# Kernel tuning notes

Hardware: AMD Instinct MI355X
Metric: run time of the kernel (lower is better)

Reference implementation:

```python
import jax, jax.numpy as jnp
import numpy as np
from jax import lax

EPS = 1e-5  # clamp floor used in both quantizers (matches torch clamp_(min=1e-05))


def activation_quant(x):
    # per-token (per n,h,w across channel dim=1) 8-bit fake quant
    scale = 127.0 / jnp.clip(jnp.max(jnp.abs(x), axis=1, keepdims=True), EPS, None)
    return jnp.clip(jnp.round(x * scale), -128.0, 127.0) / scale


def weight_quant(w):
    # per-tensor ternary (1.58-bit) fake quant
    scale = 1.0 / jnp.clip(jnp.mean(jnp.abs(w)), EPS, None)
    return jnp.clip(jnp.round(w * scale), -1.0, 1.0) / scale


def setup_inputs() -> dict:
    key = jax.random.key(0)
    kx, kw, kb = jax.random.split(key, 3)
    N, Cin, H, W = 16, 64, 256, 256
    Cout, kh, kw_ = 64, 3, 3
    x = jax.random.normal(kx, (N, Cin, H, W), dtype=jnp.float32)
    fan_in = Cin * kh * kw_
    # kaiming-uniform-like init scale
    bound = np.sqrt(6.0 / fan_in)
    weight = jax.random.uniform(kw, (Cout, Cin, kh, kw_), dtype=jnp.float32,
                                minval=-bound, maxval=bound)
    bias = jnp.zeros((Cout,), dtype=jnp.float32)
    return {"x": x, "weight": weight, "bias": bias}


def reference(x, weight, bias):
    # straight-through estimator: value = quantized, grad flows through identity
    dqx = x - lax.stop_gradient(x - activation_quant(x))
    dqw = weight - lax.stop_gradient(weight - weight_quant(weight))
    out = lax.conv_general_dilated(
        dqx, dqw,
        window_strides=(1, 1),
        padding=((1, 1), (1, 1)),
        lhs_dilation=(1, 1),
        rhs_dilation=(1, 1),
        dimension_numbers=("NCHW", "OIHW", "NCHW"),
        feature_group_count=1,
    )
    return out + bias[None, :, None, None]
```

## Files before the change

### kernel.cpp

```cpp
#include <hip/hip_runtime.h>
#include <hip/hip_bf16.h>

typedef __attribute__((ext_vector_type(8))) short short8;
typedef __attribute__((ext_vector_type(4))) float f32x4;
typedef __attribute__((ext_vector_type(4))) int i32x4;
typedef unsigned short u16;
typedef unsigned int u32;
typedef __attribute__((ext_vector_type(8))) unsigned short u16x8;
typedef __attribute__((ext_vector_type(4))) u32 u32x4;

#define XN 16
#define XC 64
#define XH 256
#define XW 256
#define XO 64
#define CH_STRIDE (XH * XW)

#define QX_OFF    0
#define INVS_OFF  67108864
#define WBUF_OFF  71303168
#define PART_OFF  71340032
#define WM_OFF    71340288
#define WS_NEED   71340544

__global__ __launch_bounds__(256) void wq_reduce(const float* __restrict__ w,
                                                 float* __restrict__ partials) {
    __shared__ float red[4];
    const int tid = threadIdx.x;
    const int base = blockIdx.x * 576;
    float s = 0.f;
    for (int i = tid; i < 576; i += 256) s += fabsf(w[base + i]);
    #pragma unroll
    for (int off = 32; off > 0; off >>= 1) s += __shfl_down(s, off, 64);
    if ((tid & 63) == 0) red[tid >> 6] = s;
    __syncthreads();
    if (tid == 0) partials[blockIdx.x] = red[0] + red[1] + red[2] + red[3];
}

__global__ __launch_bounds__(256) void wq_tern_i8(const float* __restrict__ w,
                                                  const float* __restrict__ partials,
                                                  float* __restrict__ wm_out,
                                                  signed char* __restrict__ wbuf) {
    __shared__ float wm_sh;
    const int tid = threadIdx.x;
    if (tid == 0) {
        float tot = 0.f;
        #pragma unroll
        for (int i = 0; i < 64; ++i) tot += partials[i];
        float wm = fmaxf(tot / (float)(XO * XC * 9), 1e-5f);
        wm_sh = wm;
        if (blockIdx.x == 0) wm_out[0] = wm;
    }
    __syncthreads();
    const float wscale = 1.0f / wm_sh;

    const int idx = blockIdx.x * 256 + tid;
    const int j = idx & 15;
    const int l = (idx >> 4) & 63;
    const int m = (idx >> 10) & 3;
    const int t = idx >> 12;
    const int o = m * 16 + (l & 15);
    const int i = (l >> 4) * 16 + j;
    const int kh = t / 3, kw = t % 3;
    const float wv = w[((o * XC + i) * 3 + kh) * 3 + kw];
    const float tern = fminf(fmaxf(rintf(wv * wscale), -1.f), 1.f);
    wbuf[idx] = (signed char)(int)tern;
}

__global__ __launch_bounds__(256) void aq_i8(const float* __restrict__ x,
                                             signed char* __restrict__ qx,
                                             float* __restrict__ invs) {
    const int tid = threadIdx.x;
    const int b = blockIdx.x;
    const int n = b >> 8;

    const float* px = x + ((size_t)n << 22) + ((size_t)(b & 255) << 8) + tid;
    float vals[64];
    float amax = 0.f;
    #pragma unroll
    for (int c = 0; c < 64; ++c) {
        const float v = px[(size_t)c << 16];
        vals[c] = v;
        amax = fmaxf(amax, fabsf(v));
    }
    const float am = fmaxf(amax, 1e-5f);
    const float scale = 127.0f / am;
    invs[((size_t)b << 8) + tid] = am * (1.0f / 127.0f);

    u32 words[16];
    #pragma unroll
    for (int wk = 0; wk < 16; ++wk) {
        u32 acc = 0;
        #pragma unroll
        for (int bb = 0; bb < 4; ++bb) {
            const float q = fminf(fmaxf(rintf(vals[wk * 4 + bb] * scale), -128.f), 127.f);
            acc |= ((u32)((int)q) & 255u) << (bb * 8);
        }
        words[wk] = acc;
    }
    u32* dst = (u32*)(qx + ((((size_t)b << 8) + tid) << 6));
    #pragma unroll
    for (int i = 0; i < 4; ++i) {
        *reinterpret_cast<u32x4*>(dst + i * 4) =
            (u32x4){words[i * 4], words[i * 4 + 1], words[i * 4 + 2], words[i * 4 + 3]};
    }
}

__global__ __launch_bounds__(256, 3) void conv_i8(const signed char* __restrict__ qx,
                                                  const float* __restrict__ invs,
                                                  const signed char* __restrict__ wbuf,
                                                  const float* __restrict__ wm_ptr,
                                                  const float* __restrict__ bias,
                                                  float* __restrict__ out) {
    const int tid = threadIdx.x;
    const int bid = (blockIdx.x & 7) * 1024 + (blockIdx.x >> 3);
    const int n      = bid >> 9;
    const int rem    = bid & 511;
    const int rowgrp = rem >> 3;
    const int w0     = (rem & 7) << 5;
    const int wv     = tid >> 6;
    const int gh_out = (rowgrp << 2) + wv;
    const int lane = tid & 63;
    const int l15 = lane & 15;
    const int lg  = lane >> 4;

    const float wm = wm_ptr[0];

    const signed char* qn = qx + ((size_t)n << 22);
    const float*       in = invs + ((size_t)n << 16);

    int gwc[2][3]; bool cok[2][3];
    #pragma unroll
    for (int nt = 0; nt < 2; ++nt)
        #pragma unroll
        for (int dw = 0; dw < 3; ++dw) {
            const int gw = w0 + nt * 16 + l15 + dw - 1;
            cok[nt][dw] = (gw >= 0) & (gw < XW);
            gwc[nt][dw] = min(max(gw, 0), XW - 1);
        }

    i32x4 B[9][2];
    float IV[9][2];
    #pragma unroll
    for (int dh = 0; dh < 3; ++dh) {
        const int gh = gh_out + dh - 1;
        const bool rok = (gh >= 0) & (gh < XH);
        const int ghc = min(max(gh, 0), XH - 1);
        const signed char* qrow = qn + ((size_t)ghc << 14);
        const float*       irow = in + (ghc << 8);
        #pragma unroll
        for (int dw = 0; dw < 3; ++dw) {
            #pragma unroll
            for (int nt = 0; nt < 2; ++nt) {
                const int c = gwc[nt][dw];
                B[dh * 3 + dw][nt] =
                    *reinterpret_cast<const i32x4*>(qrow + (c << 6) + (lg << 4));
                IV[dh * 3 + dw][nt] = (rok & cok[nt][dw]) ? irow[c] : 0.f;
            }
        }
    }
    __builtin_amdgcn_sched_barrier(0);

    f32x4 acc[4][2];
    #pragma unroll
    for (int m = 0; m < 4; ++m) {
        acc[m][0] = (f32x4){0.f, 0.f, 0.f, 0.f};
        acc[m][1] = (f32x4){0.f, 0.f, 0.f, 0.f};
    }

    #pragma unroll
    for (int t = 0; t < 9; ++t) {
        #pragma unroll
        for (int m = 0; m < 4; ++m) {
            const i32x4 af = *reinterpret_cast<const i32x4*>(
                wbuf + (((t << 2) + m) << 10) + (lane << 4));
            #pragma unroll
            for (int nt = 0; nt < 2; ++nt) {
                i32x4 tap = __builtin_amdgcn_mfma_i32_16x16x64_i8(
                    af, B[t][nt], (i32x4){0, 0, 0, 0}, 0, 0, 0);
                f32x4 tf;
                tf[0] = (float)tap[0]; tf[1] = (float)tap[1];
                tf[2] = (float)tap[2]; tf[3] = (float)tap[3];
                acc[m][nt] += tf * IV[t][nt];
            }
        }
    }

    #pragma unroll
    for (int m = 0; m < 4; ++m) {
        #pragma unroll
        for (int r = 0; r < 4; ++r) {
            const int o = (m << 4) + (lg << 2) + r;
            const float bz = bias[o];
            float* orow = out + ((((size_t)n << 6) + o) << 16) + (gh_out << 8) + w0;
            __builtin_nontemporal_store(fmaf(acc[m][0][r], wm, bz), orow + l15);
            __builtin_nontemporal_store(fmaf(acc[m][1][r], wm, bz), orow + 16 + l15);
        }
    }
}

#define HALO_W 34
#define NPIX 340

__global__ __launch_bounds__(256) void wq_kernel(const float* __restrict__ w,
                                                 float* __restrict__ wm_out,
                                                 u16* __restrict__ wbuf) {
    __shared__ float red[4];
    __shared__ float wm_sh;
    const int tid = threadIdx.x;

    float s = 0.f;
    for (int i = tid; i < XO * XC * 9; i += 256) s += fabsf(w[i]);
    #pragma unroll
    for (int off = 32; off > 0; off >>= 1) s += __shfl_down(s, off, 64);
    if ((tid & 63) == 0) red[tid >> 6] = s;
    __syncthreads();
    if (tid == 0) {
        float tot = red[0] + red[1] + red[2] + red[3];
        float wm = fmaxf(tot / (float)(XO * XC * 9), 1e-5f);
        wm_out[0] = wm;
        wm_sh = wm;
    }
    __syncthreads();
    const float wscale = 1.0f / wm_sh;

    for (int idx = tid; idx < XO * XC * 9; idx += 256) {
        const int j = idx & 7;
        const int l = (idx >> 3) & 63;
        const int c = (idx >> 9) & 1;
        const int m = (idx >> 10) & 3;
        const int t = idx >> 12;
        const int o = m * 16 + (l & 15);
        const int i = c * 32 + (l >> 4) * 8 + j;
        const int kh = t / 3, kw = t % 3;
        const float wv = w[((o * XC + i) * 3 + kh) * 3 + kw];
        const float tern = fminf(fmaxf(rintf(wv * wscale), -1.f), 1.f);
        wbuf[idx] = (u16)(__float_as_uint(tern) >> 16);
    }
}

__global__ __launch_bounds__(256) void conv_kernel(const float* __restrict__ x,
                                                   const u16* __restrict__ wbuf,
                                                   const float* __restrict__ wm_ptr,
                                                   const float* __restrict__ bias,
                                                   float* __restrict__ out) {
    __shared__ __align__(16) u16 q_lds[NPIX * 64];
    __shared__ float invs_lds[NPIX];
    __shared__ float bias_lds[XO];

    const int tid = threadIdx.x;
    const int bid = blockIdx.x;
    const int n   = bid >> 8;
    const int rem = bid & 255;
    const int h0  = (rem >> 3) << 3;
    const int w0  = (rem & 7) << 5;

    if (tid < XO) bias_lds[tid] = bias[tid];

    #pragma unroll 1
    for (int p = tid; p < NPIX; p += 256) {
        const int hr = p / HALO_W;
        const int cl = p - hr * HALO_W;
        const int gh = h0 + hr - 1;
        const int gw = w0 + cl - 1;
        const bool ok = (gh >= 0) & (gh < XH) & (gw >= 0) & (gw < XW);

        float vals[64];
        float amax = 0.f;
        if (ok) {
            const float* px = x + (size_t)n * (XC * CH_STRIDE) + (size_t)gh * XW + gw;
            #pragma unroll
            for (int c = 0; c < 64; ++c) {
                const float v = px[(size_t)c * CH_STRIDE];
                vals[c] = v;
                amax = fmaxf(amax, fabsf(v));
            }
        } else {
            #pragma unroll
            for (int c = 0; c < 64; ++c) vals[c] = 0.f;
        }
        const float am    = fmaxf(amax, 1e-5f);
        const float scale = 127.0f / am;
        invs_lds[p] = ok ? (1.0f / scale) : 0.0f;

        const int sw = (p & 7) << 3;
        #pragma unroll
        for (int cb = 0; cb < 8; ++cb) {
            u16x8 pk;
            #pragma unroll
            for (int j = 0; j < 8; ++j) {
                const float q = fminf(fmaxf(rintf(vals[cb * 8 + j] * scale), -128.f), 127.f);
                pk[j] = (u16)(__float_as_uint(q) >> 16);
            }
            *reinterpret_cast<u16x8*>(&q_lds[p * 64 + ((cb * 8) ^ sw)]) = pk;
        }
    }
    __syncthreads();

    const int lane = tid & 63;
    const int wv   = tid >> 6;
    const int l15  = lane & 15;
    const int lg   = lane >> 4;

    f32x4 acc[4][4];
    #pragma unroll
    for (int m = 0; m < 4; ++m)
        #pragma unroll
        for (int nt = 0; nt < 4; ++nt) acc[m][nt] = (f32x4){0.f, 0.f, 0.f, 0.f};

    const float wm = wm_ptr[0];

    #pragma unroll
    for (int t = 0; t < 9; ++t) {
        const int dh = t / 3, dw = t % 3;

        short8 afr[4][2];
        #pragma unroll
        for (int m = 0; m < 4; ++m)
            #pragma unroll
            for (int c = 0; c < 2; ++c)
                afr[m][c] = *reinterpret_cast<const short8*>(
                    wbuf + ((((t * 4 + m) * 2 + c) * 64 + lane) * 8));

        #pragma unroll
        for (int nt = 0; nt < 4; ++nt) {
            const int rl  = 2 * wv + (nt >> 1);
            const int pix = (rl + dh) * HALO_W + (nt & 1) * 16 + l15 + dw;
            const int sw  = (pix & 7) << 3;
            const u16* qp = &q_lds[pix * 64];
            const short8 b0 = *reinterpret_cast<const short8*>(qp + ((lg * 8) ^ sw));
            const short8 b1 = *reinterpret_cast<const short8*>(qp + ((32 + lg * 8) ^ sw));
            const float  iv = invs_lds[pix];
            #pragma unroll
            for (int m = 0; m < 4; ++m) {
                f32x4 tap = (f32x4){0.f, 0.f, 0.f, 0.f};
                tap = __builtin_amdgcn_mfma_f32_16x16x32_bf16(afr[m][0], b0, tap, 0, 0, 0);
                tap = __builtin_amdgcn_mfma_f32_16x16x32_bf16(afr[m][1], b1, tap, 0, 0, 0);
                acc[m][nt] += tap * iv;
            }
        }
    }

    #pragma unroll
    for (int m = 0; m < 4; ++m) {
        #pragma unroll
        for (int nt = 0; nt < 4; ++nt) {
            const int rl = 2 * wv + (nt >> 1);
            const int gh = h0 + rl;
            const int gw = w0 + (nt & 1) * 16 + l15;
            #pragma unroll
            for (int r = 0; r < 4; ++r) {
                const int o = m * 16 + lg * 4 + r;
                const float v = wm * acc[m][nt][r] + bias_lds[o];
                out[(((size_t)n * XO + o) * XH + gh) * XW + gw] = v;
            }
        }
    }
}

extern "C" void kernel_launch(void* const* d_in, const int* in_sizes, int n_in,
                              void* d_out, int out_size, void* d_ws, size_t ws_size,
                              hipStream_t stream) {
    const float* x    = (const float*)d_in[0];
    const float* w    = (const float*)d_in[1];
    const float* bias = (const float*)d_in[2];
    float* out = (float*)d_out;

    if (ws_size >= (size_t)WS_NEED) {
        signed char* qx       = (signed char*)d_ws;
        float*       invsb    = (float*)((char*)d_ws + INVS_OFF);
        signed char* wbuf     = (signed char*)((char*)d_ws + WBUF_OFF);
        float*       partials = (float*)((char*)d_ws + PART_OFF);
        float*       wm       = (float*)((char*)d_ws + WM_OFF);

        wq_reduce<<<64, 256, 0, stream>>>(w, partials);
        wq_tern_i8<<<144, 256, 0, stream>>>(w, partials, wm, wbuf);
        aq_i8<<<XN * 256, 256, 0, stream>>>(x, qx, invsb);
        conv_i8<<<XN * 512, 256, 0, stream>>>(qx, invsb, wbuf, wm, bias, out);
    } else {
        float* wsf  = (float*)d_ws;
        u16*   wbuf = (u16*)((char*)d_ws + 64);
        wq_kernel<<<1, 256, 0, stream>>>(w, wsf, wbuf);
        conv_kernel<<<XN * 256, 256, 0, stream>>>(x, wbuf, wsf, bias, out);
    }
}
```

Measured before the change: 195.8 us.

## Compute two output rows per wave and stage epilogue through LDS for vector stores

Each wave now computes two adjacent output rows, so it loads four input rows instead of six and reuses each weight fragment across both rows. The grid is halved to match. The epilogue writes results into a padded LDS tile, then issues 16-byte nontemporal global stores instead of scalar ones. In exchange, register pressure goes up (occupancy hint drops from 3 to 2 blocks) and about 73 KB of LDS per block is added, which may limit occupancy.

```diff
diff --git a/kernel.cpp b/kernel.cpp
--- a/kernel.cpp
+++ b/kernel.cpp
@@ -106,25 +106,25 @@
     }
 }
 
-__global__ __launch_bounds__(256, 3) void conv_i8(const signed char* __restrict__ qx,
+__global__ __launch_bounds__(256, 2) void conv_i8(const signed char* __restrict__ qx,
                                                   const float* __restrict__ invs,
                                                   const signed char* __restrict__ wbuf,
                                                   const float* __restrict__ wm_ptr,
                                                   const float* __restrict__ bias,
                                                   float* __restrict__ out) {
-    const int tid = threadIdx.x;
-    const int bid = (blockIdx.x & 7) * 1024 + (blockIdx.x >> 3);
-    const int n      = bid >> 9;
-    const int rem    = bid & 511;
+    __shared__ float eplds[4][2][64][36];
+
+    const int tid = threadIdx.x;
+    const int bid = (blockIdx.x & 7) * 512 + (blockIdx.x >> 3);
+    const int n      = bid >> 8;
+    const int rem    = bid & 255;
     const int rowgrp = rem >> 3;
     const int w0     = (rem & 7) << 5;
     const int wv     = tid >> 6;
-    const int gh_out = (rowgrp << 2) + wv;
+    const int gh0    = (rowgrp << 3) + (wv << 1);
     const int lane = tid & 63;
     const int l15 = lane & 15;
     const int lg  = lane >> 4;
-
-    const float wm = wm_ptr[0];
 
     const signed char* qn = qx + ((size_t)n << 22);
     const float*       in = invs + ((size_t)n << 16);
@@ -139,11 +139,11 @@
             gwc[nt][dw] = min(max(gw, 0), XW - 1);
         }
 
-    i32x4 B[9][2];
-    float IV[9][2];
-    #pragma unroll
-    for (int dh = 0; dh < 3; ++dh) {
-        const int gh = gh_out + dh - 1;
+    i32x4 B[4][3][2];
+    float IV[4][3][2];
+    #pragma unroll
+    for (int w = 0; w < 4; ++w) {
+        const int gh = gh0 + w - 1;
         const bool rok = (gh >= 0) & (gh < XH);
         const int ghc = min(max(gh, 0), XH - 1);
         const signed char* qrow = qn + ((size_t)ghc << 14);
@@ -153,48 +153,86 @@
             #pragma unroll
             for (int nt = 0; nt < 2; ++nt) {
                 const int c = gwc[nt][dw];
-                B[dh * 3 + dw][nt] =
-                    *reinterpret_cast<const i32x4*>(qrow + (c << 6) + (lg << 4));
-                IV[dh * 3 + dw][nt] = (rok & cok[nt][dw]) ? irow[c] : 0.f;
-            }
-        }
-    }
+                B[w][dw][nt] = *reinterpret_cast<const i32x4*>(qrow + (c << 6) + (lg << 4));
+                IV[w][dw][nt] = (rok & cok[nt][dw]) ? irow[c] : 0.f;
+            }
+        }
+    }
+    #pragma unroll
+    for (int w = 0; w < 4; ++w)
+        #pragma unroll
+        for (int dw = 0; dw < 3; ++dw)
+            #pragma unroll
+            for (int nt = 0; nt < 2; ++nt) {
+                asm volatile("" : "+v"(B[w][dw][nt]));
+                asm volatile("" : "+v"(IV[w][dw][nt]));
+            }
     __builtin_amdgcn_sched_barrier(0);
 
-    f32x4 acc[4][2];
-    #pragma unroll
-    for (int m = 0; m < 4; ++m) {
-        acc[m][0] = (f32x4){0.f, 0.f, 0.f, 0.f};
-        acc[m][1] = (f32x4){0.f, 0.f, 0.f, 0.f};
-    }
-
-    #pragma unroll
-    for (int t = 0; t < 9; ++t) {
-        #pragma unroll
-        for (int m = 0; m < 4; ++m) {
-            const i32x4 af = *reinterpret_cast<const i32x4*>(
-                wbuf + (((t << 2) + m) << 10) + (lane << 4));
-            #pragma unroll
-            for (int nt = 0; nt < 2; ++nt) {
-                i32x4 tap = __builtin_amdgcn_mfma_i32_16x16x64_i8(
-                    af, B[t][nt], (i32x4){0, 0, 0, 0}, 0, 0, 0);
-                f32x4 tf;
-                tf[0] = (float)tap[0]; tf[1] = (float)tap[1];
-                tf[2] = (float)tap[2]; tf[3] = (float)tap[3];
-                acc[m][nt] += tf * IV[t][nt];
-            }
-        }
-    }
-
-    #pragma unroll
-    for (int m = 0; m < 4; ++m) {
-        #pragma unroll
-        for (int r = 0; r < 4; ++r) {
-            const int o = (m << 4) + (lg << 2) + r;
-            const float bz = bias[o];
-            float* orow = out + ((((size_t)n << 6) + o) << 16) + (gh_out << 8) + w0;
-            __builtin_nontemporal_store(fmaf(acc[m][0][r], wm, bz), orow + l15);
-            __builtin_nontemporal_store(fmaf(acc[m][1][r], wm, bz), orow + 16 + l15);
+    f32x4 acc[2][4][2];
+    #pragma unroll
+    for (int ri = 0; ri < 2; ++ri)
+        #pragma unroll
+        for (int m = 0; m < 4; ++m)
+            #pragma unroll
+            for (int nt = 0; nt < 2; ++nt)
+                acc[ri][m][nt] = (f32x4){0.f, 0.f, 0.f, 0.f};
+
+    #pragma unroll
+    for (int dh = 0; dh < 3; ++dh) {
+        #pragma unroll
+        for (int dw = 0; dw < 3; ++dw) {
+            const int t = dh * 3 + dw;
+            #pragma unroll
+            for (int m = 0; m < 4; ++m) {
+                const i32x4 af = *reinterpret_cast<const i32x4*>(
+                    wbuf + (((t << 2) + m) << 10) + (lane << 4));
+                #pragma unroll
+                for (int ri = 0; ri < 2; ++ri) {
+                    const int w = ri + dh;
+                    #pragma unroll
+                    for (int nt = 0; nt < 2; ++nt) {
+                        i32x4 tap = __builtin_amdgcn_mfma_i32_16x16x64_i8(
+                            af, B[w][dw][nt], (i32x4){0, 0, 0, 0}, 0, 0, 0);
+                        f32x4 tf;
+                        tf[0] = (float)tap[0]; tf[1] = (float)tap[1];
+                        tf[2] = (float)tap[2]; tf[3] = (float)tap[3];
+                        acc[ri][m][nt] += tf * IV[w][dw][nt];
+                    }
+                }
+            }
+        }
+    }
+
+    const float wm = wm_ptr[0];
+    float bias_v[4][4];
+    #pragma unroll
+    for (int m = 0; m < 4; ++m)
+        #pragma unroll
+        for (int r = 0; r < 4; ++r)
+            bias_v[m][r] = bias[(m << 4) + (lg << 2) + r];
+
+    #pragma unroll
+    for (int ri = 0; ri < 2; ++ri)
+        #pragma unroll
+        for (int m = 0; m < 4; ++m)
+            #pragma unroll
+            for (int nt = 0; nt < 2; ++nt)
+                #pragma unroll
+                for (int r = 0; r < 4; ++r)
+                    eplds[wv][ri][(m << 4) + (lg << 2) + r][(nt << 4) + l15] =
+                        fmaf(acc[ri][m][nt][r], wm, bias_v[m][r]);
+
+    #pragma unroll
+    for (int ri = 0; ri < 2; ++ri) {
+        const int gh = gh0 + ri;
+        #pragma unroll
+        for (int j = 0; j < 8; ++j) {
+            const int o   = (j << 3) + (lane >> 3);
+            const int px0 = (lane & 7) << 2;
+            const f32x4 v = *reinterpret_cast<const f32x4*>(&eplds[wv][ri][o][px0]);
+            float* dst = out + ((((size_t)n << 6) + o) << 16) + (gh << 8) + w0 + px0;
+            __builtin_nontemporal_store(v, reinterpret_cast<f32x4*>(dst));
         }
     }
 }
@@ -376,7 +414,7 @@
         wq_reduce<<<64, 256, 0, stream>>>(w, partials);
         wq_tern_i8<<<144, 256, 0, stream>>>(w, partials, wm, wbuf);
         aq_i8<<<XN * 256, 256, 0, stream>>>(x, qx, invsb);
-        conv_i8<<<XN * 512, 256, 0, stream>>>(qx, invsb, wbuf, wm, bias, out);
+        conv_i8<<<XN * 256, 256, 0, stream>>>(qx, invsb, wbuf, wm, bias, out);
     } else {
         float* wsf  = (float*)d_ws;
         u16*   wbuf = (u16*)((char*)d_ws + 64);
```

After: 165.2 us. -15.6%, faster.

## Stage conv epilogue through LDS for 16-byte stores and force early loads

Applied to the files above, without the earlier changes.

The conv epilogue now writes the accumulators into a per-wave LDS tile and reads them back so each lane issues 16-byte vectorized nontemporal stores instead of scalar 4-byte stores. Input and scale loads are now issued through inline asm global loads with an explicit full vmcnt wait, so all loads are in flight together before the MFMA loop. This adds about 36 KB of LDS per block, which may limit occupancy. The inline asm also takes load scheduling away from the compiler.

```diff
diff --git a/kernel.cpp b/kernel.cpp
--- a/kernel.cpp
+++ b/kernel.cpp
@@ -22,6 +22,17 @@
 #define PART_OFF  71340032
 #define WM_OFF    71340288
 #define WS_NEED   71340544
+
+__device__ __forceinline__ i32x4 gload16(const void* p) {
+    i32x4 r;
+    asm volatile("global_load_dwordx4 %0, %1, off" : "=v"(r) : "v"(p) : "memory");
+    return r;
+}
+__device__ __forceinline__ float gload4(const void* p) {
+    float r;
+    asm volatile("global_load_dword %0, %1, off" : "=v"(r) : "v"(p) : "memory");
+    return r;
+}
 
 __global__ __launch_bounds__(256) void wq_reduce(const float* __restrict__ w,
                                                  float* __restrict__ partials) {
@@ -112,6 +123,8 @@
                                                   const float* __restrict__ wm_ptr,
                                                   const float* __restrict__ bias,
                                                   float* __restrict__ out) {
+    __shared__ float eplds[4][64][36];
+
     const int tid = threadIdx.x;
     const int bid = (blockIdx.x & 7) * 1024 + (blockIdx.x >> 3);
     const int n      = bid >> 9;
@@ -119,12 +132,10 @@
     const int rowgrp = rem >> 3;
     const int w0     = (rem & 7) << 5;
     const int wv     = tid >> 6;
-    const int gh_out = (rowgrp << 2) + wv;
+    const int gh     = (rowgrp << 2) + wv;
     const int lane = tid & 63;
     const int l15 = lane & 15;
     const int lg  = lane >> 4;
-
-    const float wm = wm_ptr[0];
 
     const signed char* qn = qx + ((size_t)n << 22);
     const float*       in = invs + ((size_t)n << 16);
@@ -139,27 +150,36 @@
             gwc[nt][dw] = min(max(gw, 0), XW - 1);
         }
 
-    i32x4 B[9][2];
-    float IV[9][2];
+    i32x4 B[3][3][2];
+    float IVr[3][3][2];
+    bool  rokv[3];
     #pragma unroll
     for (int dh = 0; dh < 3; ++dh) {
-        const int gh = gh_out + dh - 1;
-        const bool rok = (gh >= 0) & (gh < XH);
-        const int ghc = min(max(gh, 0), XH - 1);
+        const int ghi = gh + dh - 1;
+        rokv[dh] = (ghi >= 0) & (ghi < XH);
+        const int ghc = min(max(ghi, 0), XH - 1);
         const signed char* qrow = qn + ((size_t)ghc << 14);
         const float*       irow = in + (ghc << 8);
         #pragma unroll
-        for (int dw = 0; dw < 3; ++dw) {
+        for (int dw = 0; dw < 3; ++dw)
             #pragma unroll
             for (int nt = 0; nt < 2; ++nt) {
                 const int c = gwc[nt][dw];
-                B[dh * 3 + dw][nt] =
-                    *reinterpret_cast<const i32x4*>(qrow + (c << 6) + (lg << 4));
-                IV[dh * 3 + dw][nt] = (rok & cok[nt][dw]) ? irow[c] : 0.f;
-            }
-        }
-    }
+                B[dh][dw][nt]   = gload16(qrow + (c << 6) + (lg << 4));
+                IVr[dh][dw][nt] = gload4(irow + c);
+            }
+    }
+    asm volatile("s_waitcnt vmcnt(0)" ::: "memory");
     __builtin_amdgcn_sched_barrier(0);
+
+    float IV[3][3][2];
+    #pragma unroll
+    for (int dh = 0; dh < 3; ++dh)
+        #pragma unroll
+        for (int dw = 0; dw < 3; ++dw)
+            #pragma unroll
+            for (int nt = 0; nt < 2; ++nt)
+                IV[dh][dw][nt] = (rokv[dh] & cok[nt][dw]) ? IVr[dh][dw][nt] : 0.f;
 
     f32x4 acc[4][2];
     #pragma unroll
@@ -169,33 +189,46 @@
     }
 
     #pragma unroll
-    for (int t = 0; t < 9; ++t) {
-        #pragma unroll
-        for (int m = 0; m < 4; ++m) {
-            const i32x4 af = *reinterpret_cast<const i32x4*>(
-                wbuf + (((t << 2) + m) << 10) + (lane << 4));
-            #pragma unroll
-            for (int nt = 0; nt < 2; ++nt) {
-                i32x4 tap = __builtin_amdgcn_mfma_i32_16x16x64_i8(
-                    af, B[t][nt], (i32x4){0, 0, 0, 0}, 0, 0, 0);
-                f32x4 tf;
-                tf[0] = (float)tap[0]; tf[1] = (float)tap[1];
-                tf[2] = (float)tap[2]; tf[3] = (float)tap[3];
-                acc[m][nt] += tf * IV[t][nt];
-            }
-        }
-    }
-
-    #pragma unroll
-    for (int m = 0; m < 4; ++m) {
-        #pragma unroll
-        for (int r = 0; r < 4; ++r) {
-            const int o = (m << 4) + (lg << 2) + r;
-            const float bz = bias[o];
-            float* orow = out + ((((size_t)n << 6) + o) << 16) + (gh_out << 8) + w0;
-            __builtin_nontemporal_store(fmaf(acc[m][0][r], wm, bz), orow + l15);
-            __builtin_nontemporal_store(fmaf(acc[m][1][r], wm, bz), orow + 16 + l15);
-        }
+    for (int dh = 0; dh < 3; ++dh) {
+        #pragma unroll
+        for (int dw = 0; dw < 3; ++dw) {
+            const int t = dh * 3 + dw;
+            #pragma unroll
+            for (int m = 0; m < 4; ++m) {
+                const i32x4 af = *reinterpret_cast<const i32x4*>(
+                    wbuf + (((t << 2) + m) << 10) + (lane << 4));
+                #pragma unroll
+                for (int nt = 0; nt < 2; ++nt) {
+                    i32x4 tap = __builtin_amdgcn_mfma_i32_16x16x64_i8(
+                        af, B[dh][dw][nt], (i32x4){0, 0, 0, 0}, 0, 0, 0);
+                    f32x4 tf;
+                    tf[0] = (float)tap[0]; tf[1] = (float)tap[1];
+                    tf[2] = (float)tap[2]; tf[3] = (float)tap[3];
+                    acc[m][nt] += tf * IV[dh][dw][nt];
+                }
+            }
+        }
+    }
+
+    const float wm = wm_ptr[0];
+    #pragma unroll
+    for (int m = 0; m < 4; ++m)
+        #pragma unroll
+        for (int nt = 0; nt < 2; ++nt)
+            #pragma unroll
+            for (int r = 0; r < 4; ++r) {
+                const int o = (m << 4) + (lg << 2) + r;
+                eplds[wv][o][(nt << 4) + l15] =
+                    fmaf(acc[m][nt][r], wm, bias[o]);
+            }
+
+    #pragma unroll
+    for (int j = 0; j < 8; ++j) {
+        const int o   = (j << 3) + (lane >> 3);
+        const int px0 = (lane & 7) << 2;
+        const f32x4 v = *reinterpret_cast<const f32x4*>(&eplds[wv][o][px0]);
+        float* dst = out + ((((size_t)n << 6) + o) << 16) + (gh << 8) + w0 + px0;
+        __builtin_nontemporal_store(v, reinterpret_cast<f32x4*>(dst));
     }
 }
 
```

Result: faster. 177.4 us (-9.4%).
